# Performance work log

Hardware: AMD Instinct MI355X
Metric: run time of the kernel (lower is better)

## Reference

```python
import jax, jax.numpy as jnp
import numpy as np

B, N, D, E, H = 8, 2048, 1024, 8, 4096
CAP_FACTOR = 1.25   # capacity_factor_train
THRESHOLD = 0.2     # second_threshold_train
LOSS_COEF = 0.01
MIN_CAP = 4
EPS = 1e-9


def setup_inputs() -> dict:
    key = jax.random.key(0)
    ks = jax.random.split(key, 5)
    return {
        "hidden_states": jax.random.normal(ks[0], (B, N, D), jnp.float32),
        "wg": jax.random.normal(ks[1], (D, E), jnp.float32) * 0.02,
        "w1": jax.random.normal(ks[2], (E, D, H), jnp.float32) * 0.02,
        "b1": jnp.zeros((E, H), jnp.float32),
        "w2": jax.random.normal(ks[3], (E, H, D), jnp.float32) * 0.02,
        "b2": jnp.zeros((E, D), jnp.float32),
        "rand_probs": jax.random.uniform(ks[4], (B, N), jnp.float32),
    }


def _top2_gating(x, wg, rand_probs):
    # GShard-style top-2 gating with 'random' second policy and capacity limit.
    dt = x.dtype
    n = x.shape[-2]
    e = wg.shape[-1]
    raw = jax.nn.softmax(jnp.einsum('bnd,de->bne', x, wg), axis=-1)  # [b,n,e]
    idx1 = jnp.argmax(raw, axis=-1)
    gate1 = jnp.max(raw, axis=-1)
    mask1 = jax.nn.one_hot(idx1, e, dtype=dt)
    raw2 = raw * (1.0 - mask1)
    idx2 = jnp.argmax(raw2, axis=-1)
    gate2 = jnp.max(raw2, axis=-1)
    mask2 = jax.nn.one_hot(idx2, e, dtype=dt)
    denom = gate1 + gate2 + EPS
    gate1 = gate1 / denom
    gate2 = gate2 / denom
    # load-balancing loss (computed before capacity truncation)
    density1 = jnp.mean(mask1, axis=-2)          # [b,e]
    density1_proxy = jnp.mean(raw, axis=-2)      # [b,e]
    loss = jnp.mean(density1_proxy * density1) * (e * e)
    # second policy == 'random': keep 2nd expert w.p. ~ gate2/threshold
    mask2 = mask2 * (rand_probs < (gate2 / max(THRESHOLD, EPS)))[..., None].astype(dt)
    capacity = max(min(n, int(n * CAP_FACTOR / e)), MIN_CAP)
    # exclusive cumsum over tokens -> position within expert
    pos1 = (jnp.cumsum(mask1, axis=-2) - mask1) * mask1
    mask1 = mask1 * (pos1 < capacity).astype(dt)
    mask1_count = jnp.sum(mask1, axis=-2, keepdims=True)
    mask1_flat = jnp.sum(mask1, axis=-1)
    pos1 = jnp.sum(pos1, axis=-1)
    gate1 = gate1 * mask1_flat
    pos2 = (jnp.cumsum(mask2, axis=-2) - mask2 + mask1_count) * mask2
    mask2 = mask2 * (pos2 < capacity).astype(dt)
    mask2_flat = jnp.sum(mask2, axis=-1)
    pos2 = jnp.sum(pos2, axis=-1)
    gate2 = gate2 * mask2_flat
    # combine tensor [b,n,e,c]; out-of-range positions one_hot to zeros
    oh_p1 = jax.nn.one_hot(pos1.astype(jnp.int32), capacity, dtype=dt)
    oh_p2 = jax.nn.one_hot(pos2.astype(jnp.int32), capacity, dtype=dt)
    combine = ((gate1 * mask1_flat)[..., None, None]
               * jax.nn.one_hot(idx1, e, dtype=dt)[..., None] * oh_p1[..., None, :]
               + (gate2 * mask2_flat)[..., None, None]
               * jax.nn.one_hot(idx2, e, dtype=dt)[..., None] * oh_p2[..., None, :])
    dispatch = (combine > 0).astype(dt)
    return dispatch, combine, loss


def reference(hidden_states, wg, w1, b1, w2, b2, rand_probs):
    dispatch, combine, loss = _top2_gating(hidden_states, wg, rand_probs)
    # dispatch tokens to per-expert capacity buffers: [e,b,c,d]
    ei = jnp.einsum('bnd,bnec->ebcd', hidden_states, dispatch)
    # per-expert FFN (grouped GEMMs)
    h = jax.nn.gelu(jnp.einsum('ebcd,edh->ebch', ei, w1) + b1[:, None, None, :],
                    approximate=False)
    eo = jnp.einsum('ebch,ehd->ebcd', h, w2) + b2[:, None, None, :]
    # combine back to token order with gate weights
    out = jnp.einsum('ebcd,bnec->bnd', eo, combine)
    # dropout is identity (output_dropout_prob=0.0 / eval mode)
    return out, loss * LOSS_COEF
```

## Files before the change

### kernel.cpp

```cpp
#include <hip/hip_runtime.h>
#include <hip/hip_bf16.h>
#include <math.h>

#define BB 8
#define NN 2048
#define DD 1024
#define EE 8
#define HH 4096
#define CAP 320
#define NTOK (BB*NN)
#define MBC (BB*CAP)

typedef __bf16 bf16x8 __attribute__((ext_vector_type(8)));
typedef float f32x4 __attribute__((ext_vector_type(4)));
typedef unsigned u32x4 __attribute__((ext_vector_type(4)));
typedef unsigned short u16x4 __attribute__((ext_vector_type(4)));
typedef unsigned short u16x8v __attribute__((ext_vector_type(8)));
typedef unsigned short u16;

__device__ __forceinline__ u16 f2bf(float f) {
    unsigned u = __builtin_bit_cast(unsigned, f);
    u += 0x7FFFu + ((u >> 16) & 1u);
    return (u16)(u >> 16);
}

__device__ __forceinline__ void async_cp16(const void* g, void* l) {
    __builtin_amdgcn_global_load_lds((const __attribute__((address_space(1))) void*)g,
                                     (__attribute__((address_space(3))) void*)l,
                                     16, 0, 0);
}

__device__ __forceinline__ float gelu_fast(float v) {
    float u = v * (0.7978845608f + 0.0356774081f * v * v);
    u = fminf(fmaxf(u, -30.0f), 30.0f);
    float ex = __expf(-2.0f * u);
    float th = (1.0f - ex) / (1.0f + ex);
    return 0.5f * v * (1.0f + th);
}

__global__ void MoE_zero_stats(float* stats) {
    if (threadIdx.x < 128) stats[threadIdx.x] = 0.0f;
}

__global__ __launch_bounds__(256) void MoE_gating(
    const float* __restrict__ x, const float* __restrict__ wg,
    const float* __restrict__ rp,
    int* __restrict__ i1o, int* __restrict__ i2o,
    float* __restrict__ g1o, float* __restrict__ g2o, int* __restrict__ keepo,
    float* __restrict__ proxy, float* __restrict__ cnt1,
    float* __restrict__ out_zero)
{
    __shared__ float wgT[8*1024];
    __shared__ float sprox[8];
    __shared__ float scnt[8];
    int tid = threadIdx.x;
    {
        f32x4 z = {0,0,0,0};
        f32x4* dst = (f32x4*)(out_zero + (size_t)blockIdx.x * 4 * DD);
        #pragma unroll
        for (int i = 0; i < 4; i++) dst[tid + 256*i] = z;
    }
    {
        int d0 = tid*4;
        #pragma unroll
        for (int j = 0; j < 4; j++) {
            int d = d0 + j;
            f32x4 a = *(const f32x4*)(wg + d*8);
            f32x4 b = *(const f32x4*)(wg + d*8 + 4);
            wgT[0*1024+d]=a[0]; wgT[1*1024+d]=a[1]; wgT[2*1024+d]=a[2]; wgT[3*1024+d]=a[3];
            wgT[4*1024+d]=b[0]; wgT[5*1024+d]=b[1]; wgT[6*1024+d]=b[2]; wgT[7*1024+d]=b[3];
        }
    }
    if (tid < 8) { sprox[tid] = 0.0f; scnt[tid] = 0.0f; }
    __syncthreads();

    int wid = tid >> 6, lane = tid & 63;
    int tok = blockIdx.x*4 + wid;
    int b = tok >> 11;
    const float* xr = x + (size_t)tok * DD;

    double acc[8];
    #pragma unroll
    for (int e = 0; e < 8; e++) acc[e] = 0.0;
    for (int i = 0; i < 16; i++) {
        float xv = xr[i*64 + lane];
        #pragma unroll
        for (int e = 0; e < 8; e++)
            acc[e] += (double)xv * (double)wgT[e*1024 + i*64 + lane];
    }
    #pragma unroll
    for (int e = 0; e < 8; e++) {
        double v = acc[e];
        for (int off = 32; off; off >>= 1) v += __shfl_down(v, off, 64);
        acc[e] = v;
    }
    if (lane == 0) {
        float l[8];
        #pragma unroll
        for (int e = 0; e < 8; e++) l[e] = (float)acc[e];
        int i1 = 0;
        #pragma unroll
        for (int e = 1; e < 8; e++) if (l[e] > l[i1]) i1 = e;
        int i2 = (i1 == 0) ? 1 : 0;
        #pragma unroll
        for (int e = 0; e < 8; e++) if (e != i1 && l[e] > l[i2]) i2 = e;
        float mx = l[i1], p[8], s = 0.0f;
        #pragma unroll
        for (int e = 0; e < 8; e++) { p[e] = expf(l[e] - mx); s += p[e]; }
        float inv = 1.0f / s;
        #pragma unroll
        for (int e = 0; e < 8; e++) p[e] *= inv;
        float gate1 = p[i1], gate2 = p[i2];
        float denom = gate1 + gate2 + 1e-9f;
        float g1 = gate1 / denom, g2 = gate2 / denom;
        int keep = (rp[tok] < g2 / 0.2f) ? 1 : 0;
        i1o[tok] = i1; i2o[tok] = i2; g1o[tok] = g1; g2o[tok] = g2; keepo[tok] = keep;
        #pragma unroll
        for (int e = 0; e < 8; e++) atomicAdd(&sprox[e], p[e]);
        atomicAdd(&scnt[i1], 1.0f);
    }
    __syncthreads();
    if (tid < 8) {
        atomicAdd(&proxy[b*8 + tid], sprox[tid]);
        atomicAdd(&cnt1[b*8 + tid], scnt[tid]);
    }
}

__global__ __launch_bounds__(256) void MoE_scan(
    const int* __restrict__ i1, const int* __restrict__ i2, const int* __restrict__ keep,
    const float* __restrict__ g1, const float* __restrict__ g2,
    int* __restrict__ slot_token, float* __restrict__ slot_gate)
{
    int b = blockIdx.x, t = threadIdx.x;
    __shared__ unsigned long long s0[256], s1[256];
    for (int s = t; s < EE*CAP; s += 256) {
        int e = s / CAP, c = s % CAP;
        slot_token[(e*BB + b)*CAP + c] = -1;
    }
    int base = b*NN + t*8;

    int e1v[8];
    unsigned long long u0 = 0, u1 = 0;
    #pragma unroll
    for (int j = 0; j < 8; j++) {
        int e = i1[base + j]; e1v[j] = e;
        if (e < 4) u0 += 1ull << (e*16); else u1 += 1ull << ((e-4)*16);
    }
    s0[t] = u0; s1[t] = u1;
    __syncthreads();
    for (int off = 1; off < 256; off <<= 1) {
        unsigned long long a0 = 0, a1 = 0;
        if (t >= off) { a0 = s0[t-off]; a1 = s1[t-off]; }
        __syncthreads();
        s0[t] += a0; s1[t] += a1;
        __syncthreads();
    }
    unsigned long long t0 = s0[255], t1 = s1[255];
    unsigned long long x0 = s0[t] - u0, x1 = s1[t] - u1;
    int run[8], mc[8];
    #pragma unroll
    for (int e = 0; e < 8; e++) {
        run[e] = (int)((e < 4 ? (x0 >> (e*16)) : (x1 >> ((e-4)*16))) & 0xFFFF);
        int tot = (int)((e < 4 ? (t0 >> (e*16)) : (t1 >> ((e-4)*16))) & 0xFFFF);
        mc[e] = tot < CAP ? tot : CAP;
    }
    #pragma unroll
    for (int j = 0; j < 8; j++) {
        int e = e1v[j];
        int p = run[e]++;
        if (p < CAP) {
            slot_token[(e*BB + b)*CAP + p] = t*8 + j;
            slot_gate[(e*BB + b)*CAP + p] = g1[base + j];
        }
    }
    __syncthreads();

    int e2v[8], kv[8];
    u0 = 0; u1 = 0;
    #pragma unroll
    for (int j = 0; j < 8; j++) {
        int e = i2[base + j]; e2v[j] = e;
        int k = keep[base + j]; kv[j] = k;
        if (k) { if (e < 4) u0 += 1ull << (e*16); else u1 += 1ull << ((e-4)*16); }
    }
    s0[t] = u0; s1[t] = u1;
    __syncthreads();
    for (int off = 1; off < 256; off <<= 1) {
        unsigned long long a0 = 0, a1 = 0;
        if (t >= off) { a0 = s0[t-off]; a1 = s1[t-off]; }
        __syncthreads();
        s0[t] += a0; s1[t] += a1;
        __syncthreads();
    }
    x0 = s0[t] - u0; x1 = s1[t] - u1;
    #pragma unroll
    for (int e = 0; e < 8; e++)
        run[e] = mc[e] + (int)((e < 4 ? (x0 >> (e*16)) : (x1 >> ((e-4)*16))) & 0xFFFF);
    #pragma unroll
    for (int j = 0; j < 8; j++) {
        if (kv[j]) {
            int e = e2v[j];
            int p = run[e]++;
            if (p < CAP) {
                slot_token[(e*BB + b)*CAP + p] = t*8 + j;
                slot_gate[(e*BB + b)*CAP + p] = g2[base + j];
            }
        }
    }
}

__global__ __launch_bounds__(256) void MoE_dispatch(
    const float* __restrict__ x, const int* __restrict__ slot_token,
    u16* __restrict__ Abuf)
{
    int tid = threadIdx.x, wid = tid >> 6, lane = tid & 63;
    int slot = blockIdx.x*4 + wid;
    int b = (slot % (BB*CAP)) / CAP;
    int tok = slot_token[slot];
    u16* dst = Abuf + (size_t)slot * DD;
    if (tok >= 0) {
        const float* src = x + ((size_t)b*NN + tok) * DD;
        #pragma unroll
        for (int i = 0; i < 4; i++) {
            f32x4 v = *(const f32x4*)(src + (lane + 64*i)*4);
            u16x4 w = { f2bf(v[0]), f2bf(v[1]), f2bf(v[2]), f2bf(v[3]) };
            *(u16x4*)(dst + (lane + 64*i)*4) = w;
        }
    } else {
        u16x4 z = {0,0,0,0};
        #pragma unroll
        for (int i = 0; i < 4; i++) *(u16x4*)(dst + (lane + 64*i)*4) = z;
    }
}

__global__ __launch_bounds__(256) void MoE_transpose_bf16(
    const float* __restrict__ in, u16* __restrict__ out,
    int R, int C, int rTiles, int cTiles)
{
    int tilesPerE = rTiles * cTiles;
    int e = blockIdx.x / tilesPerE;
    int t = blockIdx.x % tilesPerE;
    int r0 = (t / cTiles) * 64, c0 = (t % cTiles) * 64;
    const float* ip = in + (size_t)e * R * C;
    u16* op = out + (size_t)e * R * C;
    __shared__ float T[64*65];
    int tid = threadIdx.x;
    {
        int rr = tid >> 4, cx = tid & 15;
        #pragma unroll
        for (int i = 0; i < 4; i++) {
            int r = rr + i*16;
            f32x4 v = *(const f32x4*)(ip + (size_t)(r0 + r)*C + c0 + cx*4);
            float* d = T + r*65 + cx*4;
            d[0]=v[0]; d[1]=v[1]; d[2]=v[2]; d[3]=v[3];
        }
    }
    __syncthreads();
    {
        int cw = tid >> 3, rx = tid & 7;
        int r = rx*8;
        #pragma unroll
        for (int i = 0; i < 2; i++) {
            int c = cw + i*32;
            u16x8v w;
            #pragma unroll
            for (int jj = 0; jj < 8; jj++) w[jj] = f2bf(T[(r+jj)*65 + c]);
            *(u16x8v*)(op + (size_t)(c0 + c)*R + r0 + r) = w;
        }
    }
}

template <int MODE>
__global__ __launch_bounds__(256, 3) void MoE_gemm_bt(
    const u16* __restrict__ Aall, const u16* __restrict__ Ball,
    void* __restrict__ Call, const float* __restrict__ biasAll,
    const int* __restrict__ slot_token, const float* __restrict__ slot_gate,
    int M, int N, int K, int mTiles, int nTiles)
{
    int bid = blockIdx.x;
    int e = bid & 7;
    int i = bid >> 3;
    const int GM = 8;
    int group = i / (GM*nTiles);
    int gm = mTiles - group*GM; if (gm > GM) gm = GM;
    int rem = i - group*GM*nTiles;
    int n_ = rem / gm;
    int mm = rem % gm;
    if (n_ & 1) mm = gm - 1 - mm;
    int m0 = (group*GM + mm) * 128;
    int n0 = n_ * 128;

    const u16* A  = Aall + (size_t)e * M * K;
    const u16* Bm = Ball + (size_t)e * N * K;
    const float* bias = biasAll + (size_t)e * N;

    __shared__ u16 sA[128*64];
    __shared__ u16 sB[128*64];

    int tid = threadIdx.x;
    int lane = tid & 63, wid = tid >> 6;
    int wm = wid & 1, wn = wid >> 1;
    int l16 = lane & 15, quad = lane >> 4;

    const u16* gA[4]; const u16* gB[4]; u16* dA[4]; u16* dB[4];
    #pragma unroll
    for (int l = 0; l < 4; l++) {
        int ch = l*256 + tid;
        int row = ch >> 3;
        int gc  = (ch & 7) ^ (row & 7);
        gA[l] = A  + (size_t)(m0 + row)*K + gc*8;
        gB[l] = Bm + (size_t)(n0 + row)*K + gc*8;
        dA[l] = sA + (size_t)(l*256 + (tid & ~63)) * 8;
        dB[l] = sB + (size_t)(l*256 + (tid & ~63)) * 8;
    }

    int rbaseA = (wm*64 + l16)*64;
    int rbaseB = (wn*64 + l16)*64;
    int sw = l16 & 7;
    int swz0 = ((0*4 + quad) ^ sw) * 8;
    int swz1 = ((1*4 + quad) ^ sw) * 8;

    f32x4 acc[4][4] = {};
    int ksteps = K / 64;
    for (int kk = 0; kk < ksteps; ++kk) {
        #pragma unroll
        for (int l = 0; l < 4; l++) {
            async_cp16(gA[l], dA[l]);
            async_cp16(gB[l], dB[l]);
            gA[l] += 64; gB[l] += 64;
        }
        __syncthreads();
        #pragma unroll
        for (int h = 0; h < 2; h++) {
            int swz = h ? swz1 : swz0;
            bf16x8 av[4], bv[4];
            #pragma unroll
            for (int i2 = 0; i2 < 4; i2++) av[i2] = __builtin_bit_cast(bf16x8, *(const u32x4*)(sA + rbaseA + i2*1024 + swz));
            #pragma unroll
            for (int j = 0; j < 4; j++) bv[j] = __builtin_bit_cast(bf16x8, *(const u32x4*)(sB + rbaseB + j*1024 + swz));
            #pragma unroll
            for (int i2 = 0; i2 < 4; i2++)
                #pragma unroll
                for (int j = 0; j < 4; j++)
                    acc[i2][j] = __builtin_amdgcn_mfma_f32_16x16x32_bf16(av[i2], bv[j], acc[i2][j], 0, 0, 0);
        }
        __syncthreads();
    }

    if (MODE == 0) {
        u16* C = (u16*)Call + (size_t)e * M * N;
        #pragma unroll
        for (int i2 = 0; i2 < 4; i2++) {
            int m = m0 + wm*64 + i2*16 + quad*4;
            #pragma unroll
            for (int j = 0; j < 4; j++) {
                int n = n0 + wn*64 + j*16 + l16;
                float bn = bias[n];
                #pragma unroll
                for (int r = 0; r < 4; r++) {
                    float v = acc[i2][j][r] + bn;
                    C[(size_t)(m + r)*N + n] = f2bf(gelu_fast(v));
                }
            }
        }
    } else {
        float* outp = (float*)Call;
        float bn[4];
        #pragma unroll
        for (int j = 0; j < 4; j++) bn[j] = bias[n0 + wn*64 + j*16 + l16];
        #pragma unroll
        for (int i2 = 0; i2 < 4; i2++) {
            #pragma unroll
            for (int r = 0; r < 4; r++) {
                int mr = m0 + wm*64 + i2*16 + quad*4 + r;
                int bb = mr / CAP;
                int cc = mr - bb*CAP;
                int sidx = (e*BB + bb)*CAP + cc;
                int tok = slot_token[sidx];
                if (tok < 0) continue;
                float g = slot_gate[sidx];
                float* orow = outp + ((size_t)bb*NN + tok)*DD + n0 + wn*64 + l16;
                #pragma unroll
                for (int j = 0; j < 4; j++)
                    atomicAdd(orow + j*16, g * (acc[i2][j][r] + bn[j]));
            }
        }
    }
}

__global__ void MoE_loss(const float* __restrict__ proxy, const float* __restrict__ cnt,
                         float* __restrict__ out)
{
    int t = threadIdx.x;
    float v = proxy[t] * cnt[t];
    for (int off = 32; off; off >>= 1) v += __shfl_down(v, off, 64);
    if (t == 0) out[0] = v * (0.01f / ((float)NN * (float)NN));
}

extern "C" void kernel_launch(void* const* d_in, const int* in_sizes, int n_in,
                              void* d_out, int out_size, void* d_ws, size_t ws_size,
                              hipStream_t stream) {
    const float* x  = (const float*)d_in[0];
    const float* wg = (const float*)d_in[1];
    const float* w1 = (const float*)d_in[2];
    const float* b1 = (const float*)d_in[3];
    const float* w2 = (const float*)d_in[4];
    const float* b2 = (const float*)d_in[5];
    const float* rp = (const float*)d_in[6];
    float* out = (float*)d_out;

    char* w = (char*)d_ws;
    auto alloc = [&](size_t bytes) -> char* {
        char* p = w; w += (bytes + 255) & ~(size_t)255; return p;
    };
    u16*   w1b  = (u16*)alloc((size_t)2*EE*DD*HH);
    u16*   w2b  = (u16*)alloc((size_t)2*EE*HH*DD);
    u16*   Abuf = (u16*)alloc((size_t)2*EE*MBC*DD);
    u16*   Hbuf = (u16*)alloc((size_t)2*EE*MBC*HH);
    int*   i1   = (int*)alloc(4*NTOK);
    int*   i2   = (int*)alloc(4*NTOK);
    int*   keep = (int*)alloc(4*NTOK);
    float* g1   = (float*)alloc(4*NTOK);
    float* g2   = (float*)alloc(4*NTOK);
    int*   slot = (int*)alloc(4*EE*BB*CAP);
    float* sgate= (float*)alloc(4*EE*BB*CAP);
    float* stats = (float*)alloc(4*128);
    float* proxy = stats;
    float* cnt   = stats + 64;

    MoE_zero_stats<<<1, 128, 0, stream>>>(stats);
    MoE_transpose_bf16<<<EE*16*64, 256, 0, stream>>>(w1, w1b, 1024, 4096, 16, 64);
    MoE_transpose_bf16<<<EE*64*16, 256, 0, stream>>>(w2, w2b, 4096, 1024, 64, 16);
    MoE_gating<<<NTOK/4, 256, 0, stream>>>(x, wg, rp, i1, i2, g1, g2, keep, proxy, cnt, out);
    MoE_scan<<<BB, 256, 0, stream>>>(i1, i2, keep, g1, g2, slot, sgate);
    MoE_dispatch<<<EE*BB*CAP/4, 256, 0, stream>>>(x, slot, Abuf);
    MoE_gemm_bt<0><<<EE*20*32, 256, 0, stream>>>(Abuf, w1b, Hbuf, b1, nullptr, nullptr, MBC, HH, DD, 20, 32);
    MoE_gemm_bt<1><<<EE*20*8, 256, 0, stream>>>(Hbuf, w2b, out, b2, slot, sgate, MBC, DD, HH, 20, 8);
    MoE_loss<<<1, 64, 0, stream>>>(proxy, cnt, out + (size_t)NTOK*DD);
}
```

Before: 859.9 us.

## Use 256x128 GEMM tiles with 512 threads, split-K for second GEMM, fuse prep kernels

The grouped GEMM tile grows from 128x128 with 4 waves to 256x128 with 8 waves, so each B tile loaded into LDS is reused across more rows. The down-projection GEMM uses split-K by 2 and applies the bias only in the first split, which keeps the grid large enough now that tiles are bigger; its atomic output accumulation already supports this. The stats zeroing and the two weight transpose kernels are merged into one launch. The costs are more LDS per block, which may lower occupancy relative to the declared launch bounds, and twice as many atomics in the second GEMM.

```diff
diff --git a/kernel.cpp b/kernel.cpp
--- a/kernel.cpp
+++ b/kernel.cpp
@@ -38,8 +38,48 @@
     return 0.5f * v * (1.0f + th);
 }
 
-__global__ void MoE_zero_stats(float* stats) {
-    if (threadIdx.x < 128) stats[threadIdx.x] = 0.0f;
+__global__ __launch_bounds__(256) void MoE_prep(
+    const float* __restrict__ w1, u16* __restrict__ w1b,
+    const float* __restrict__ w2, u16* __restrict__ w2b,
+    float* __restrict__ stats)
+{
+    int bid = blockIdx.x;
+    int tid = threadIdx.x;
+    if (bid == 0 && tid < 128) stats[tid] = 0.0f;
+
+    const float* in; u16* outp; int R, C, cTiles; int t;
+    if (bid < 8192) { in = w1; outp = w1b; R = 1024; C = 4096; cTiles = 64; t = bid; }
+    else            { in = w2; outp = w2b; R = 4096; C = 1024; cTiles = 16; t = bid - 8192; }
+    int tilesPerE = (R/64) * cTiles;
+    int e = t / tilesPerE;
+    int tt = t % tilesPerE;
+    int r0 = (tt / cTiles) * 64, c0 = (tt % cTiles) * 64;
+    const float* ip = in + (size_t)e * R * C;
+    u16* op = outp + (size_t)e * R * C;
+    __shared__ float T[64*65];
+    {
+        int rr = tid >> 4, cx = tid & 15;
+        #pragma unroll
+        for (int i = 0; i < 4; i++) {
+            int r = rr + i*16;
+            f32x4 v = *(const f32x4*)(ip + (size_t)(r0 + r)*C + c0 + cx*4);
+            float* d = T + r*65 + cx*4;
+            d[0]=v[0]; d[1]=v[1]; d[2]=v[2]; d[3]=v[3];
+        }
+    }
+    __syncthreads();
+    {
+        int cw = tid >> 3, rx = tid & 7;
+        int r = rx*8;
+        #pragma unroll
+        for (int i = 0; i < 2; i++) {
+            int c = cw + i*32;
+            u16x8v wv;
+            #pragma unroll
+            for (int jj = 0; jj < 8; jj++) wv[jj] = f2bf(T[(r+jj)*65 + c]);
+            *(u16x8v*)(op + (size_t)(c0 + c)*R + r0 + r) = wv;
+        }
+    }
 }
 
 __global__ __launch_bounds__(256) void MoE_gating(
@@ -233,102 +273,74 @@
     }
 }
 
-__global__ __launch_bounds__(256) void MoE_transpose_bf16(
-    const float* __restrict__ in, u16* __restrict__ out,
-    int R, int C, int rTiles, int cTiles)
-{
-    int tilesPerE = rTiles * cTiles;
-    int e = blockIdx.x / tilesPerE;
-    int t = blockIdx.x % tilesPerE;
-    int r0 = (t / cTiles) * 64, c0 = (t % cTiles) * 64;
-    const float* ip = in + (size_t)e * R * C;
-    u16* op = out + (size_t)e * R * C;
-    __shared__ float T[64*65];
-    int tid = threadIdx.x;
-    {
-        int rr = tid >> 4, cx = tid & 15;
-        #pragma unroll
-        for (int i = 0; i < 4; i++) {
-            int r = rr + i*16;
-            f32x4 v = *(const f32x4*)(ip + (size_t)(r0 + r)*C + c0 + cx*4);
-            float* d = T + r*65 + cx*4;
-            d[0]=v[0]; d[1]=v[1]; d[2]=v[2]; d[3]=v[3];
-        }
-    }
-    __syncthreads();
-    {
-        int cw = tid >> 3, rx = tid & 7;
-        int r = rx*8;
-        #pragma unroll
-        for (int i = 0; i < 2; i++) {
-            int c = cw + i*32;
-            u16x8v w;
-            #pragma unroll
-            for (int jj = 0; jj < 8; jj++) w[jj] = f2bf(T[(r+jj)*65 + c]);
-            *(u16x8v*)(op + (size_t)(c0 + c)*R + r0 + r) = w;
-        }
-    }
-}
-
-template <int MODE>
-__global__ __launch_bounds__(256, 3) void MoE_gemm_bt(
+template <int MODE, int SPLITK>
+__global__ __launch_bounds__(512, 4) void MoE_gemm_bt(
     const u16* __restrict__ Aall, const u16* __restrict__ Ball,
     void* __restrict__ Call, const float* __restrict__ biasAll,
     const int* __restrict__ slot_token, const float* __restrict__ slot_gate,
-    int M, int N, int K, int mTiles, int nTiles)
+    int M, int N, int K, int mTiles, int nTiles, int GM)
 {
     int bid = blockIdx.x;
     int e = bid & 7;
-    int i = bid >> 3;
-    const int GM = 8;
+    int idx = bid >> 3;
+    int tilesPer = mTiles * nTiles;
+    int sk = (SPLITK > 1) ? (idx / tilesPer) : 0;
+    int i  = (SPLITK > 1) ? (idx % tilesPer) : idx;
     int group = i / (GM*nTiles);
     int gm = mTiles - group*GM; if (gm > GM) gm = GM;
     int rem = i - group*GM*nTiles;
     int n_ = rem / gm;
     int mm = rem % gm;
     if (n_ & 1) mm = gm - 1 - mm;
-    int m0 = (group*GM + mm) * 128;
+    int m0 = (group*GM + mm) * 256;
     int n0 = n_ * 128;
-
-    const u16* A  = Aall + (size_t)e * M * K;
-    const u16* Bm = Ball + (size_t)e * N * K;
+    int Keff = K / SPLITK;
+    int k0 = sk * Keff;
+
+    const u16* A  = Aall + (size_t)e * M * K + k0;
+    const u16* Bm = Ball + (size_t)e * N * K + k0;
     const float* bias = biasAll + (size_t)e * N;
 
-    __shared__ u16 sA[128*64];
+    __shared__ u16 sA[256*64];
     __shared__ u16 sB[128*64];
 
     int tid = threadIdx.x;
     int lane = tid & 63, wid = tid >> 6;
-    int wm = wid & 1, wn = wid >> 1;
+    int wm = wid & 3, wn = wid >> 2;
     int l16 = lane & 15, quad = lane >> 4;
 
-    const u16* gA[4]; const u16* gB[4]; u16* dA[4]; u16* dB[4];
+    const u16* gA[4]; u16* dA[4];
     #pragma unroll
     for (int l = 0; l < 4; l++) {
-        int ch = l*256 + tid;
+        int ch = l*512 + tid;
         int row = ch >> 3;
         int gc  = (ch & 7) ^ (row & 7);
-        gA[l] = A  + (size_t)(m0 + row)*K + gc*8;
+        gA[l] = A + (size_t)(m0 + row)*K + gc*8;
+        dA[l] = sA + (size_t)(l*512 + (tid & ~63)) * 8;
+    }
+    const u16* gB[2]; u16* dB[2];
+    #pragma unroll
+    for (int l = 0; l < 2; l++) {
+        int ch = l*512 + tid;
+        int row = ch >> 3;
+        int gc  = (ch & 7) ^ (row & 7);
         gB[l] = Bm + (size_t)(n0 + row)*K + gc*8;
-        dA[l] = sA + (size_t)(l*256 + (tid & ~63)) * 8;
-        dB[l] = sB + (size_t)(l*256 + (tid & ~63)) * 8;
+        dB[l] = sB + (size_t)(l*512 + (tid & ~63)) * 8;
     }
 
     int rbaseA = (wm*64 + l16)*64;
     int rbaseB = (wn*64 + l16)*64;
     int sw = l16 & 7;
-    int swz0 = ((0*4 + quad) ^ sw) * 8;
-    int swz1 = ((1*4 + quad) ^ sw) * 8;
+    int swz0 = (quad ^ sw) * 8;
+    int swz1 = ((4 + quad) ^ sw) * 8;
 
     f32x4 acc[4][4] = {};
-    int ksteps = K / 64;
+    int ksteps = Keff / 64;
     for (int kk = 0; kk < ksteps; ++kk) {
         #pragma unroll
-        for (int l = 0; l < 4; l++) {
-            async_cp16(gA[l], dA[l]);
-            async_cp16(gB[l], dB[l]);
-            gA[l] += 64; gB[l] += 64;
-        }
+        for (int l = 0; l < 4; l++) { async_cp16(gA[l], dA[l]); gA[l] += 64; }
+        #pragma unroll
+        for (int l = 0; l < 2; l++) { async_cp16(gB[l], dB[l]); gB[l] += 64; }
         __syncthreads();
         #pragma unroll
         for (int h = 0; h < 2; h++) {
@@ -365,9 +377,10 @@
         }
     } else {
         float* outp = (float*)Call;
+        float bscale = (SPLITK == 1 || sk == 0) ? 1.0f : 0.0f;
         float bn[4];
         #pragma unroll
-        for (int j = 0; j < 4; j++) bn[j] = bias[n0 + wn*64 + j*16 + l16];
+        for (int j = 0; j < 4; j++) bn[j] = bias[n0 + wn*64 + j*16 + l16] * bscale;
         #pragma unroll
         for (int i2 = 0; i2 < 4; i2++) {
             #pragma unroll
@@ -428,13 +441,13 @@
     float* proxy = stats;
     float* cnt   = stats + 64;
 
-    MoE_zero_stats<<<1, 128, 0, stream>>>(stats);
-    MoE_transpose_bf16<<<EE*16*64, 256, 0, stream>>>(w1, w1b, 1024, 4096, 16, 64);
-    MoE_transpose_bf16<<<EE*64*16, 256, 0, stream>>>(w2, w2b, 4096, 1024, 64, 16);
+    MoE_prep<<<16384, 256, 0, stream>>>(w1, w1b, w2, w2b, stats);
     MoE_gating<<<NTOK/4, 256, 0, stream>>>(x, wg, rp, i1, i2, g1, g2, keep, proxy, cnt, out);
     MoE_scan<<<BB, 256, 0, stream>>>(i1, i2, keep, g1, g2, slot, sgate);
     MoE_dispatch<<<EE*BB*CAP/4, 256, 0, stream>>>(x, slot, Abuf);
-    MoE_gemm_bt<0><<<EE*20*32, 256, 0, stream>>>(Abuf, w1b, Hbuf, b1, nullptr, nullptr, MBC, HH, DD, 20, 32);
-    MoE_gemm_bt<1><<<EE*20*8, 256, 0, stream>>>(Hbuf, w2b, out, b2, slot, sgate, MBC, DD, HH, 20, 8);
+    MoE_gemm_bt<0,1><<<EE*10*32, 512, 0, stream>>>(Abuf, w1b, Hbuf, b1, nullptr, nullptr,
+                                                   MBC, HH, DD, 10, 32, 5);
+    MoE_gemm_bt<1,2><<<EE*10*8*2, 512, 0, stream>>>(Hbuf, w2b, out, b2, slot, sgate,
+                                                    MBC, DD, HH, 10, 8, 5);
     MoE_loss<<<1, 64, 0, stream>>>(proxy, cnt, out + (size_t)NTOK*DD);
 }
```

Measured after the change: 901.3 us. 1.05x slower.
